# Kernel optimization log

Hardware: AMD Instinct MI355X
Metric: run time of the kernel (lower is better)

Reference implementation:

```python
import jax, jax.numpy as jnp
import numpy as np

B, T, D_IN, H, E = 256, 512, 256, 256, 96  # batch, enc seq, input_size, hidden_size, num_embeddings


def setup_inputs() -> dict:
    key = jax.random.key(0)
    ks = jax.random.split(key, 12)
    s = 0.05
    return {
        "prev_h": jax.random.normal(ks[0], (B, H), jnp.float32),
        "prev_c": jax.random.normal(ks[1], (B, H), jnp.float32),
        "batch_H": jax.random.normal(ks[2], (B, T, D_IN), jnp.float32),
        "char_onehots": jax.random.uniform(ks[3], (B, E), jnp.float32),
        "W_i2h": jax.random.normal(ks[4], (H, D_IN), jnp.float32) * s,
        "W_h2h": jax.random.normal(ks[5], (H, H), jnp.float32) * s,
        "b_h2h": jax.random.normal(ks[6], (H,), jnp.float32) * s,
        "W_score": jax.random.normal(ks[7], (1, H), jnp.float32) * s,
        "W_ih": jax.random.normal(ks[8], (4 * H, D_IN + E), jnp.float32) * s,
        "W_hh": jax.random.normal(ks[9], (4 * H, H), jnp.float32) * s,
        "b_ih": jax.random.normal(ks[10], (4 * H,), jnp.float32) * s,
        "b_hh": jax.random.normal(ks[11], (4 * H,), jnp.float32) * s,
    }


def reference(prev_h, prev_c, batch_H, char_onehots,
              W_i2h, W_h2h, b_h2h, W_score, W_ih, W_hh, b_ih, b_hh):
    # additive attention over encoder features
    proj = jnp.einsum('btd,hd->bth', batch_H, W_i2h)          # [B,T,H]
    hid = prev_h @ W_h2h.T + b_h2h                             # [B,H]
    e = jnp.einsum('bth,oh->bto', jnp.tanh(proj + hid[:, None, :]), W_score)  # [B,T,1]
    alpha = jax.nn.softmax(e, axis=1)                          # [B,T,1]
    context = jnp.einsum('bt,btd->bd', alpha[..., 0], batch_H) # [B,D_IN]
    x = jnp.concatenate([context, char_onehots], axis=1)       # [B,D_IN+E]
    # LSTM cell step (PyTorch gate order: i, f, g, o)
    gates = x @ W_ih.T + b_ih + prev_h @ W_hh.T + b_hh         # [B,4H]
    i, f, g, o = jnp.split(gates, 4, axis=1)
    c_new = jax.nn.sigmoid(f) * prev_c + jax.nn.sigmoid(i) * jnp.tanh(g)
    h_new = jax.nn.sigmoid(o) * jnp.tanh(c_new)
    return (h_new, c_new, jnp.swapaxes(alpha, 1, 2))           # alpha -> [B,1,T]
```

## Files before the change

kernel.cpp:

```cpp
#include <hip/hip_runtime.h>

typedef __attribute__((ext_vector_type(8))) short short8;
typedef __attribute__((ext_vector_type(4))) float f32x4;

#define KPAD 40

#define WS_HID 0u
#define WS_P   262144u
#define WS_Z   786432u
#define WS_CTX 802816u
#define WS_WBF 1064960u

__device__ __forceinline__ unsigned cvtpk(float lo, float hi) {
    unsigned r;
    asm("v_cvt_pk_bf16_f32 %0, %1, %2" : "=v"(r) : "v"(lo), "v"(hi));
    return r;
}
__device__ __forceinline__ int4 pack8(float4 x0, float4 x1) {
    int4 q;
    q.x = (int)cvtpk(x0.x, x0.y);
    q.y = (int)cvtpk(x0.z, x0.w);
    q.z = (int)cvtpk(x1.x, x1.y);
    q.w = (int)cvtpk(x1.z, x1.w);
    return q;
}
__device__ __forceinline__ float tanh_fast(float x) {
    float e2 = __expf(2.f * x);
    return 1.f - 2.f * __builtin_amdgcn_rcpf(e2 + 1.f);
}
__device__ __forceinline__ float sigmoid_fast(float x) {
    return __builtin_amdgcn_rcpf(1.f + __expf(-x));
}
__device__ __forceinline__ void gload16(const void* g, void* l) {
    __builtin_amdgcn_global_load_lds((const __attribute__((address_space(1))) void*)g,
                                     (__attribute__((address_space(3))) void*)l, 16, 0, 0);
}

__global__ __launch_bounds__(256) void k_prep(
    const float* __restrict__ prev_h, const float* __restrict__ W_i2h,
    const float* __restrict__ W_h2h, const float* __restrict__ b_h2h,
    float* __restrict__ hid, int4* __restrict__ Wbf)
{
    int bid = blockIdx.x, tid = threadIdx.x;
    if (bid < 256) {
        __shared__ float ph[256];
        ph[tid] = prev_h[bid * 256 + tid];
        __syncthreads();
        float acc = b_h2h[tid];
        const float4* w = (const float4*)(W_h2h + tid * 256);
        #pragma unroll 8
        for (int k4 = 0; k4 < 64; ++k4) {
            float4 ww = w[k4];
            acc += ww.x * ph[k4*4+0] + ww.y * ph[k4*4+1] + ww.z * ph[k4*4+2] + ww.w * ph[k4*4+3];
        }
        hid[bid * 256 + tid] = acc;
    } else {
        int u = (bid - 256) * 256 + tid;
        int cf = u >> 9, ks = (u >> 6) & 7;
        int n = cf * 16 + (u & 15);
        int k0 = ks * 32 + ((u >> 4) & 3) * 8;
        float4 x0 = *(const float4*)(W_i2h + n * 256 + k0);
        float4 x1 = *(const float4*)(W_i2h + n * 256 + k0 + 4);
        Wbf[u] = pack8(x0, x1);
    }
}

__global__ __launch_bounds__(512, 2) void k_e(
    const float* __restrict__ BH, const int4* __restrict__ Wbf,
    const float* __restrict__ hid, const float* __restrict__ Wsc,
    float* __restrict__ p_out, float* __restrict__ zbuf)
{
    __shared__ short Blds[65536];
    __shared__ float zsh[8];

    const int tid = threadIdx.x;
    const int lane = tid & 63;
    const int w8 = tid >> 6;
    const int l15 = lane & 15, lg = lane >> 4;
    const int b = blockIdx.x;

    float4 la[16];
    auto issueA = [&](int tile) {
        const float* base = BH + ((size_t)b * 512 + tile * 16 + l15) * 256 + lg * 8;
        #pragma unroll
        for (int ks = 0; ks < 8; ++ks) {
            la[2 * ks]     = *(const float4*)(base + ks * 32);
            la[2 * ks + 1] = *(const float4*)(base + ks * 32 + 4);
        }
    };
    issueA(w8);

    {
        const char* g = (const char*)Wbf;
        char* l = (char*)Blds;
        #pragma unroll
        for (int rnd = 0; rnd < 16; ++rnd)
            gload16(g + rnd * 8192 + tid * 16, l + rnd * 8192 + tid * 16);
    }

    float wsv[16], hd[16];
    #pragma unroll
    for (int cf = 0; cf < 16; ++cf) {
        wsv[cf] = Wsc[cf * 16 + l15];
        hd[cf]  = hid[b * 256 + cf * 16 + l15];
    }
    __syncthreads();

    float zacc = 0.f;
    for (int ti = 0; ti < 4; ++ti) {
        const int tile = ti * 8 + w8;
        f32x4 acc[16];
        #pragma unroll
        for (int cf = 0; cf < 16; ++cf) acc[cf] = (f32x4){0.f, 0.f, 0.f, 0.f};

        #pragma unroll
        for (int ks = 0; ks < 8; ++ks) {
            short8 af; *(int4*)&af = pack8(la[2 * ks], la[2 * ks + 1]);
            #pragma unroll
            for (int cf = 0; cf < 16; ++cf) {
                short8 bfr = *(const short8*)&Blds[(cf * 512 + ks * 64 + lane) * 8];
                acc[cf] = __builtin_amdgcn_mfma_f32_16x16x32_bf16(af, bfr, acc[cf], 0, 0, 0);
            }
        }
        if (ti < 3) issueA(tile + 8);

        float esum[4] = {0.f, 0.f, 0.f, 0.f};
        #pragma unroll
        for (int cf = 0; cf < 16; ++cf)
            #pragma unroll
            for (int r = 0; r < 4; ++r)
                esum[r] += wsv[cf] * tanh_fast(acc[cf][r] + hd[cf]);
        #pragma unroll
        for (int r = 0; r < 4; ++r) {
            float s = esum[r];
            s += __shfl_xor(s, 1); s += __shfl_xor(s, 2);
            s += __shfl_xor(s, 4); s += __shfl_xor(s, 8);
            esum[r] = s;
        }
        float ps = 0.f, p4r[4];
        #pragma unroll
        for (int r = 0; r < 4; ++r) { p4r[r] = __expf(esum[r]); ps += p4r[r]; }
        if (l15 == 0) {
            #pragma unroll
            for (int r = 0; r < 4; ++r)
                p_out[b * 512 + tile * 16 + lg * 4 + r] = p4r[r];
        }
        ps += __shfl_xor(ps, 16); ps += __shfl_xor(ps, 32);
        zacc += ps;
    }
    if (lane == 0) zsh[w8] = zacc;
    __syncthreads();
    if (tid == 0) {
        float z = 0.f;
        #pragma unroll
        for (int i = 0; i < 8; ++i) z += zsh[i];
        zbuf[b] = z;
    }
}

__global__ __launch_bounds__(256) void k_ctx(
    const float* __restrict__ p, const float* __restrict__ zbuf,
    const float* __restrict__ BH, float* __restrict__ alpha, float* __restrict__ ctx)
{
    __shared__ float pl[512];
    int b = blockIdx.x, t = threadIdx.x;
    pl[t] = p[b * 512 + t];
    pl[256 + t] = p[b * 512 + 256 + t];
    __syncthreads();
    float inv = 1.f / zbuf[b];
    alpha[b * 512 + t] = pl[t] * inv;
    alpha[b * 512 + 256 + t] = pl[256 + t] * inv;
    const float* bh = BH + (size_t)b * 512 * 256 + t;
    float acc = 0.f;
    #pragma unroll 16
    for (int tt = 0; tt < 512; ++tt) acc += pl[tt] * bh[(size_t)tt * 256];
    ctx[b * 256 + t] = acc * inv;
}

__global__ __launch_bounds__(256) void k_gates_lstm(
    const float* __restrict__ ctx, const float* __restrict__ onehot,
    const float* __restrict__ prev_h, const float* __restrict__ W_ih,
    const float* __restrict__ W_hh, const float* __restrict__ b_ih,
    const float* __restrict__ b_hh, const float* __restrict__ prev_c,
    float* __restrict__ out)
{
    __shared__ char smem[20800];
    short* AlB = (short*)smem;
    short* BlB = (short*)smem + 5120;
    const int tid = threadIdx.x;
    const int lane = tid & 63;
    const int w = tid >> 6;
    const int l15 = lane & 15, lg = lane >> 4;
    const int rb = blockIdx.x * 64;
    const int hb = blockIdx.y;

    f32x4 acc[4];
    #pragma unroll
    for (int j = 0; j < 4; j++) acc[j] = (f32x4){0.f, 0.f, 0.f, 0.f};

    const int arow = tid >> 2, akg = tid & 3;
    const int rg = rb + arow;
    const int bn = tid >> 2, bq = tid & 3;
    const int np_ = hb * 64 + bn, hh_ = np_ >> 2, gg_ = np_ & 3;
    const float* wih_row = W_ih + (size_t)(gg_ * 256 + hh_) * 352;
    const float* whh_row = W_hh + (size_t)(gg_ * 256 + hh_) * 256;

    auto stageAB = [&](int kc, int bu) {
        int k0 = kc * 32 + akg * 8;
        const float4* pa;
        if (k0 < 256)      pa = (const float4*)(ctx    + rg * 256 + k0);
        else if (k0 < 352) pa = (const float4*)(onehot + rg * 96  + (k0 - 256));
        else               pa = (const float4*)(prev_h + rg * 256 + (k0 - 352));
        float4 x0 = pa[0], x1 = pa[1];
        *(int4*)&AlB[bu * 2560 + arow * KPAD + akg * 8] = pack8(x0, x1);
        int kb = kc * 32 + bq * 8;
        const float* pb = (kb < 352) ? (wih_row + kb) : (whh_row + (kb - 352));
        float4 y0 = *(const float4*)pb, y1 = *(const float4*)(pb + 4);
        *(int4*)&BlB[bu * 2560 + bn * KPAD + bq * 8] = pack8(y0, y1);
    };

    stageAB(0, 0);
    __syncthreads();

    for (int kc = 0; kc < 19; ++kc) {
        int cur = kc & 1;
        short8 af = *(const short8*)&AlB[cur * 2560 + (w * 16 + l15) * KPAD + lg * 8];
        short8 bfr[4];
        #pragma unroll
        for (int cf = 0; cf < 4; cf++)
            bfr[cf] = *(const short8*)&BlB[cur * 2560 + (cf * 16 + l15) * KPAD + lg * 8];
        if (kc < 18) stageAB(kc + 1, cur ^ 1);
        #pragma unroll
        for (int cf = 0; cf < 4; cf++)
            acc[cf] = __builtin_amdgcn_mfma_f32_16x16x32_bf16(af, bfr[cf], acc[cf], 0, 0, 0);
        __syncthreads();
    }

    float* Gt = (float*)smem;
    #pragma unroll
    for (int cf = 0; cf < 4; cf++) {
        int col = cf * 16 + l15;
        int np = hb * 64 + col;
        int hg = np >> 2, g = np & 3;
        float bias = b_ih[g * 256 + hg] + b_hh[g * 256 + hg];
        #pragma unroll
        for (int r = 0; r < 4; r++)
            Gt[(w * 16 + lg * 4 + r) * 65 + col] = acc[cf][r] + bias;
    }
    __syncthreads();

    #pragma unroll
    for (int it = 0; it < 4; ++it) {
        int elem = it * 256 + tid;
        int row = elem >> 4, hl = elem & 15;
        float gi = Gt[row * 65 + hl * 4 + 0];
        float gf = Gt[row * 65 + hl * 4 + 1];
        float gg = Gt[row * 65 + hl * 4 + 2];
        float go = Gt[row * 65 + hl * 4 + 3];
        int bg = rb + row, hglob = hb * 16 + hl;
        float cv = sigmoid_fast(gf) * prev_c[bg * 256 + hglob] + sigmoid_fast(gi) * tanh_fast(gg);
        out[bg * 256 + hglob] = sigmoid_fast(go) * tanh_fast(cv);
        out[65536 + bg * 256 + hglob] = cv;
    }
}

extern "C" void kernel_launch(void* const* d_in, const int* in_sizes, int n_in,
                              void* d_out, int out_size, void* d_ws, size_t ws_size,
                              hipStream_t stream) {
    (void)in_sizes; (void)n_in; (void)out_size; (void)ws_size;
    const float* prev_h  = (const float*)d_in[0];
    const float* prev_c  = (const float*)d_in[1];
    const float* batch_H = (const float*)d_in[2];
    const float* onehot  = (const float*)d_in[3];
    const float* W_i2h   = (const float*)d_in[4];
    const float* W_h2h   = (const float*)d_in[5];
    const float* b_h2h   = (const float*)d_in[6];
    const float* W_score = (const float*)d_in[7];
    const float* W_ih    = (const float*)d_in[8];
    const float* W_hh    = (const float*)d_in[9];
    const float* b_ih    = (const float*)d_in[10];
    const float* b_hh    = (const float*)d_in[11];

    char* ws = (char*)d_ws;
    float* hid   = (float*)(ws + WS_HID);
    float* p     = (float*)(ws + WS_P);
    float* zbuf  = (float*)(ws + WS_Z);
    float* ctx   = (float*)(ws + WS_CTX);
    int4*  Wbf   = (int4*)(ws + WS_WBF);

    float* out = (float*)d_out;
    float* alpha = out + 131072;

    hipLaunchKernelGGL(k_prep,       dim3(288),    dim3(256), 0, stream,
                       prev_h, W_i2h, W_h2h, b_h2h, hid, Wbf);
    hipLaunchKernelGGL(k_e,          dim3(256),    dim3(512), 0, stream,
                       batch_H, Wbf, hid, W_score, p, zbuf);
    hipLaunchKernelGGL(k_ctx,        dim3(256),    dim3(256), 0, stream,
                       p, zbuf, batch_H, alpha, ctx);
    hipLaunchKernelGGL(k_gates_lstm, dim3(4, 16),  dim3(256), 0, stream,
                       ctx, onehot, prev_h, W_ih, W_hh, b_ih, b_hh, prev_c, out);
}
```

Baseline: 84.06 us.

## Fuse context reduction into attention kernel reusing loaded encoder tiles

```diff
diff --git a/kernel.cpp b/kernel.cpp
--- a/kernel.cpp
+++ b/kernel.cpp
@@ -6,10 +6,8 @@
 #define KPAD 40
 
 #define WS_HID 0u
-#define WS_P   262144u
-#define WS_Z   786432u
-#define WS_CTX 802816u
-#define WS_WBF 1064960u
+#define WS_CTX 262144u
+#define WS_WBF 524288u
 
 __device__ __forceinline__ unsigned cvtpk(float lo, float hi) {
     unsigned r;
@@ -23,6 +21,10 @@
     q.z = (int)cvtpk(x1.x, x1.y);
     q.w = (int)cvtpk(x1.z, x1.w);
     return q;
+}
+__device__ __forceinline__ float bf2f(unsigned s) {
+    union { float f; unsigned u; } v; v.u = s << 16;
+    return v.f;
 }
 __device__ __forceinline__ float tanh_fast(float x) {
     float e2 = __expf(2.f * x);
@@ -65,12 +67,15 @@
     }
 }
 
-__global__ __launch_bounds__(512, 2) void k_e(
+__global__ __launch_bounds__(512, 2) void k_attn(
     const float* __restrict__ BH, const int4* __restrict__ Wbf,
     const float* __restrict__ hid, const float* __restrict__ Wsc,
-    float* __restrict__ p_out, float* __restrict__ zbuf)
+    float* __restrict__ alpha, float* __restrict__ ctx)
 {
     __shared__ short Blds[65536];
+    __shared__ float hdl[256], wscl[256];
+    __shared__ float pl8[8][16];
+    __shared__ float r8[8][256];
     __shared__ float zsh[8];
 
     const int tid = threadIdx.x;
@@ -79,57 +84,89 @@
     const int l15 = lane & 15, lg = lane >> 4;
     const int b = blockIdx.x;
 
-    float4 la[16];
-    auto issueA = [&](int tile) {
-        const float* base = BH + ((size_t)b * 512 + tile * 16 + l15) * 256 + lg * 8;
-        #pragma unroll
-        for (int ks = 0; ks < 8; ++ks) {
-            la[2 * ks]     = *(const float4*)(base + ks * 32);
-            la[2 * ks + 1] = *(const float4*)(base + ks * 32 + 4);
-        }
-    };
-    issueA(w8);
+    int4 la[16];
+    #define ISSUE_A(tile_)                                                          \
+        {                                                                           \
+            const float* base_ = BH + ((size_t)b * 512 + (tile_) * 16 + l15) * 256  \
+                                 + lg * 8;                                          \
+            asm volatile(                                                           \
+                "global_load_dwordx4 %0, %16, off offset:0\n"                       \
+                "global_load_dwordx4 %1, %16, off offset:16\n"                      \
+                "global_load_dwordx4 %2, %16, off offset:128\n"                     \
+                "global_load_dwordx4 %3, %16, off offset:144\n"                     \
+                "global_load_dwordx4 %4, %16, off offset:256\n"                     \
+                "global_load_dwordx4 %5, %16, off offset:272\n"                     \
+                "global_load_dwordx4 %6, %16, off offset:384\n"                     \
+                "global_load_dwordx4 %7, %16, off offset:400\n"                     \
+                "global_load_dwordx4 %8, %16, off offset:512\n"                     \
+                "global_load_dwordx4 %9, %16, off offset:528\n"                     \
+                "global_load_dwordx4 %10, %16, off offset:640\n"                    \
+                "global_load_dwordx4 %11, %16, off offset:656\n"                    \
+                "global_load_dwordx4 %12, %16, off offset:768\n"                    \
+                "global_load_dwordx4 %13, %16, off offset:784\n"                    \
+                "global_load_dwordx4 %14, %16, off offset:896\n"                    \
+                "global_load_dwordx4 %15, %16, off offset:912\n"                    \
+                : "=v"(la[0]), "=v"(la[1]), "=v"(la[2]), "=v"(la[3]),               \
+                  "=v"(la[4]), "=v"(la[5]), "=v"(la[6]), "=v"(la[7]),               \
+                  "=v"(la[8]), "=v"(la[9]), "=v"(la[10]), "=v"(la[11]),             \
+                  "=v"(la[12]), "=v"(la[13]), "=v"(la[14]), "=v"(la[15])            \
+                : "v"(base_));                                                      \
+        }
+
+    ISSUE_A(w8);
 
     {
         const char* g = (const char*)Wbf;
-        char* l = (char*)Blds;
         #pragma unroll
         for (int rnd = 0; rnd < 16; ++rnd)
-            gload16(g + rnd * 8192 + tid * 16, l + rnd * 8192 + tid * 16);
-    }
-
-    float wsv[16], hd[16];
-    #pragma unroll
-    for (int cf = 0; cf < 16; ++cf) {
-        wsv[cf] = Wsc[cf * 16 + l15];
-        hd[cf]  = hid[b * 256 + cf * 16 + l15];
-    }
+            gload16(g + rnd * 8192 + tid * 16, (char*)Blds + rnd * 8192 + tid * 16);
+    }
+    if (tid < 256) { hdl[tid] = hid[b * 256 + tid]; wscl[tid] = Wsc[tid]; }
     __syncthreads();
 
+    float ctxacc[64];
+    #pragma unroll
+    for (int i = 0; i < 64; ++i) ctxacc[i] = 0.f;
+    float p4[4][4];
     float zacc = 0.f;
+
+    #pragma unroll
     for (int ti = 0; ti < 4; ++ti) {
         const int tile = ti * 8 + w8;
-        f32x4 acc[16];
-        #pragma unroll
-        for (int cf = 0; cf < 16; ++cf) acc[cf] = (f32x4){0.f, 0.f, 0.f, 0.f};
-
+        asm volatile("s_waitcnt vmcnt(0)" ::: "memory");
+        __builtin_amdgcn_sched_barrier(0);
+        short8 af[8];
         #pragma unroll
         for (int ks = 0; ks < 8; ++ks) {
-            short8 af; *(int4*)&af = pack8(la[2 * ks], la[2 * ks + 1]);
-            #pragma unroll
-            for (int cf = 0; cf < 16; ++cf) {
-                short8 bfr = *(const short8*)&Blds[(cf * 512 + ks * 64 + lane) * 8];
-                acc[cf] = __builtin_amdgcn_mfma_f32_16x16x32_bf16(af, bfr, acc[cf], 0, 0, 0);
+            float4 f0, f1;
+            *(int4*)&f0 = la[2 * ks];
+            *(int4*)&f1 = la[2 * ks + 1];
+            *(int4*)&af[ks] = pack8(f0, f1);
+        }
+        if (ti < 3) ISSUE_A(tile + 8);
+
+        float esum[4] = {0.f, 0.f, 0.f, 0.f};
+        #pragma unroll
+        for (int h2 = 0; h2 < 2; ++h2) {
+            f32x4 acc[8];
+            #pragma unroll
+            for (int c = 0; c < 8; ++c) acc[c] = (f32x4){0.f, 0.f, 0.f, 0.f};
+            #pragma unroll
+            for (int ks = 0; ks < 8; ++ks)
+                #pragma unroll
+                for (int c = 0; c < 8; ++c)
+                    acc[c] = __builtin_amdgcn_mfma_f32_16x16x32_bf16(af[ks],
+                        *(const short8*)&Blds[(((h2 * 8 + c) * 512) + ks * 64 + lane) * 8],
+                        acc[c], 0, 0, 0);
+            #pragma unroll
+            for (int c = 0; c < 8; ++c) {
+                int col = (h2 * 8 + c) * 16 + l15;
+                float wv = wscl[col], hv = hdl[col];
+                #pragma unroll
+                for (int r = 0; r < 4; ++r)
+                    esum[r] += wv * tanh_fast(acc[c][r] + hv);
             }
         }
-        if (ti < 3) issueA(tile + 8);
-
-        float esum[4] = {0.f, 0.f, 0.f, 0.f};
-        #pragma unroll
-        for (int cf = 0; cf < 16; ++cf)
-            #pragma unroll
-            for (int r = 0; r < 4; ++r)
-                esum[r] += wsv[cf] * tanh_fast(acc[cf][r] + hd[cf]);
         #pragma unroll
         for (int r = 0; r < 4; ++r) {
             float s = esum[r];
@@ -137,44 +174,57 @@
             s += __shfl_xor(s, 4); s += __shfl_xor(s, 8);
             esum[r] = s;
         }
-        float ps = 0.f, p4r[4];
-        #pragma unroll
-        for (int r = 0; r < 4; ++r) { p4r[r] = __expf(esum[r]); ps += p4r[r]; }
-        if (l15 == 0) {
-            #pragma unroll
-            for (int r = 0; r < 4; ++r)
-                p_out[b * 512 + tile * 16 + lg * 4 + r] = p4r[r];
-        }
+        float ps = 0.f;
+        #pragma unroll
+        for (int r = 0; r < 4; ++r) { p4[ti][r] = __expf(esum[r]); ps += p4[ti][r]; }
         ps += __shfl_xor(ps, 16); ps += __shfl_xor(ps, 32);
         zacc += ps;
-    }
+        if (l15 == 0) {
+            #pragma unroll
+            for (int r = 0; r < 4; ++r) pl8[w8][lg * 4 + r] = p4[ti][r];
+        }
+        float pv = pl8[w8][l15];
+        #pragma unroll
+        for (int ks = 0; ks < 8; ++ks)
+            #pragma unroll
+            for (int j = 0; j < 8; ++j)
+                ctxacc[ks * 8 + j] += pv * bf2f((unsigned)(unsigned short)af[ks][j]);
+    }
+
     if (lane == 0) zsh[w8] = zacc;
+    #pragma unroll
+    for (int i = 0; i < 64; ++i) {
+        float s = ctxacc[i];
+        s += __shfl_xor(s, 1); s += __shfl_xor(s, 2);
+        s += __shfl_xor(s, 4); s += __shfl_xor(s, 8);
+        ctxacc[i] = s;
+    }
+    if (l15 == 0) {
+        #pragma unroll
+        for (int ks = 0; ks < 8; ++ks)
+            #pragma unroll
+            for (int j = 0; j < 8; ++j)
+                r8[w8][ks * 32 + lg * 8 + j] = ctxacc[ks * 8 + j];
+    }
     __syncthreads();
-    if (tid == 0) {
-        float z = 0.f;
-        #pragma unroll
-        for (int i = 0; i < 8; ++i) z += zsh[i];
-        zbuf[b] = z;
-    }
-}
-
-__global__ __launch_bounds__(256) void k_ctx(
-    const float* __restrict__ p, const float* __restrict__ zbuf,
-    const float* __restrict__ BH, float* __restrict__ alpha, float* __restrict__ ctx)
-{
-    __shared__ float pl[512];
-    int b = blockIdx.x, t = threadIdx.x;
-    pl[t] = p[b * 512 + t];
-    pl[256 + t] = p[b * 512 + 256 + t];
-    __syncthreads();
-    float inv = 1.f / zbuf[b];
-    alpha[b * 512 + t] = pl[t] * inv;
-    alpha[b * 512 + 256 + t] = pl[256 + t] * inv;
-    const float* bh = BH + (size_t)b * 512 * 256 + t;
-    float acc = 0.f;
-    #pragma unroll 16
-    for (int tt = 0; tt < 512; ++tt) acc += pl[tt] * bh[(size_t)tt * 256];
-    ctx[b * 256 + t] = acc * inv;
+    float Z = 0.f;
+    #pragma unroll
+    for (int i = 0; i < 8; ++i) Z += zsh[i];
+    const float inv = 1.f / Z;
+    if (l15 == 0) {
+        #pragma unroll
+        for (int ti = 0; ti < 4; ++ti)
+            #pragma unroll
+            for (int r = 0; r < 4; ++r)
+                alpha[b * 512 + (ti * 8 + w8) * 16 + lg * 4 + r] = p4[ti][r] * inv;
+    }
+    if (tid < 256) {
+        float s = 0.f;
+        #pragma unroll
+        for (int ww = 0; ww < 8; ++ww) s += r8[ww][tid];
+        ctx[b * 256 + tid] = s * inv;
+    }
+    #undef ISSUE_A
 }
 
 __global__ __launch_bounds__(256) void k_gates_lstm(
@@ -282,21 +332,17 @@
     const float* b_hh    = (const float*)d_in[11];
 
     char* ws = (char*)d_ws;
-    float* hid   = (float*)(ws + WS_HID);
-    float* p     = (float*)(ws + WS_P);
-    float* zbuf  = (float*)(ws + WS_Z);
-    float* ctx   = (float*)(ws + WS_CTX);
-    int4*  Wbf   = (int4*)(ws + WS_WBF);
+    float* hid = (float*)(ws + WS_HID);
+    float* ctx = (float*)(ws + WS_CTX);
+    int4*  Wbf = (int4*)(ws + WS_WBF);
 
     float* out = (float*)d_out;
     float* alpha = out + 131072;
 
-    hipLaunchKernelGGL(k_prep,       dim3(288),    dim3(256), 0, stream,
+    hipLaunchKernelGGL(k_prep,       dim3(288),   dim3(256), 0, stream,
                        prev_h, W_i2h, W_h2h, b_h2h, hid, Wbf);
-    hipLaunchKernelGGL(k_e,          dim3(256),    dim3(512), 0, stream,
-                       batch_H, Wbf, hid, W_score, p, zbuf);
-    hipLaunchKernelGGL(k_ctx,        dim3(256),    dim3(256), 0, stream,
-                       p, zbuf, batch_H, alpha, ctx);
-    hipLaunchKernelGGL(k_gates_lstm, dim3(4, 16),  dim3(256), 0, stream,
+    hipLaunchKernelGGL(k_attn,       dim3(256),   dim3(512), 0, stream,
+                       batch_H, Wbf, hid, W_score, alpha, ctx);
+    hipLaunchKernelGGL(k_gates_lstm, dim3(4, 16), dim3(256), 0, stream,
                        ctx, onehot, prev_h, W_ih, W_hh, b_ih, b_hh, prev_c, out);
 }
```

Result: faster. 77.64 us (-7.6%).
